# Kernel optimization log

Hardware: AMD Instinct MI355X
Metric: run time of the kernel (lower is better)

Reference implementation:

```python
import jax, jax.numpy as jnp
from jax import lax
import numpy as np

VAR0, VAR1 = 0.1, 0.2
K_TOP, T1, T2 = 5, 0.35, 0.5
ALPHA, GAMMA, BETA = 0.25, 2.0, 0.11


def point_form(b):
    # center form (cx,cy,w,h) -> corner form (x1,y1,x2,y2)
    return jnp.concatenate([b[:, :2] - b[:, 2:] / 2, b[:, :2] + b[:, 2:] / 2], axis=-1)


def jaccard(a, b):
    # a: [N,4], b: [P,4] corner boxes -> IoU [N,P]
    lt = jnp.maximum(a[:, None, :2], b[None, :, :2])
    rb = jnp.minimum(a[:, None, 2:], b[None, :, 2:])
    wh = jnp.clip(rb - lt, 0.0)
    inter = wh[..., 0] * wh[..., 1]
    area_a = ((a[:, 2] - a[:, 0]) * (a[:, 3] - a[:, 1]))[:, None]
    area_b = ((b[:, 2] - b[:, 0]) * (b[:, 3] - b[:, 1]))[None, :]
    return inter / (area_a + area_b - inter)


def encode(matched, priors):
    # matched: corner boxes [P,4], priors: center form [P,4]
    g_cxcy = ((matched[:, :2] + matched[:, 2:]) / 2 - priors[:, :2]) / (VAR0 * priors[:, 2:])
    g_wh = jnp.log((matched[:, 2:] - matched[:, :2]) / priors[:, 2:]) / VAR1
    return jnp.concatenate([g_cxcy, g_wh], axis=-1)


def decode(loc, priors):
    cxcy = priors[:, :2] + loc[:, :2] * VAR0 * priors[:, 2:]
    wh = priors[:, 2:] * jnp.exp(loc[:, 2:] * VAR1)
    return jnp.concatenate([cxcy - wh / 2, cxcy + wh / 2], axis=-1)


def _bce_logits(x, t):
    return jnp.maximum(x, 0.0) - x * t + jnp.log1p(jnp.exp(-jnp.abs(x)))


def focal_loss(logits, target, f_iou=None):
    C = logits.shape[-1]
    t = target.reshape(-1, 1)
    keep = (t >= 0.0).astype(logits.dtype)
    t = jnp.maximum(t, 0.0)
    pos = jnp.sum(t > 0.0).astype(logits.dtype)
    x = jnp.take_along_axis(logits.reshape(-1, C), t.astype(jnp.int32), axis=1)
    ce = _bce_logits(x, t)
    a = t * ALPHA + (1.0 - t) * (1.0 - ALPHA)
    p = jax.nn.sigmoid(x)
    pt = jnp.where(t == 1.0, p, 1.0 - p)
    if f_iou is not None:
        a = lax.stop_gradient(f_iou.reshape(-1, 1)) * a
    loss = a * (1.0 - pt) ** GAMMA * ce * keep
    return jnp.sum(loss) / jnp.maximum(pos, 1.0)


def smoothl1_masked(pred, target, mask):
    # equals SmoothL1Loss on the masked rows: sum(elem)/num_rows
    x = jnp.abs(pred - target)
    elem = jnp.where(x >= BETA, x - 0.5 * BETA, 0.5 * x * x / BETA)
    n = jnp.sum(mask).astype(pred.dtype)
    return jnp.sum(elem * mask[..., None].astype(pred.dtype)) / jnp.maximum(n, 1.0)


def match_image(loc_pred, tgt, priors_c, priors_pt):
    N = tgt.shape[0]
    P = priors_c.shape[0]
    truths = tgt[:, :4]
    labels = tgt[:, 4]
    iou = jaccard(truths, priors_pt)  # [N,P]
    bt_score = jnp.max(iou, axis=0)
    bt_idx = jnp.argmax(iou, axis=0).astype(jnp.int32)

    def greedy(_, st):
        m, s, ix = st
        flat = jnp.argmax(m)
        j = (flat // P).astype(jnp.int32)
        i = (flat % P).astype(jnp.int32)
        v = m.ravel()[flat]
        m = m.at[j, :].set(-1.0)
        m = m.at[:, i].set(-1.0)
        return (m, s.at[i].set(v), ix.at[i].set(j))

    _, bt_score, bt_idx = lax.fori_loop(0, N, greedy, (iou, bt_score, bt_idx))

    conf_s1 = labels[bt_idx]
    conf_s1 = jnp.where(bt_score < T1, 0.0, conf_s1)
    loc_s1 = encode(truths[bt_idx], priors_c)

    decoded = decode(lax.stop_gradient(loc_pred), priors_c)
    c_iou = jaccard(truths, decoded)  # [N,P]
    c_bp_score = jnp.max(c_iou, axis=0)
    c_bp_idx = jnp.argmax(c_iou, axis=0).astype(jnp.int32)
    c_iou = c_iou * (c_iou >= T2).astype(c_iou.dtype)
    tk_s, tk_i = lax.top_k(c_iou, K_TOP)  # per-truth top-K priors
    c_score = jnp.zeros_like(c_bp_score)

    def assign(t, st):
        cbi, cs = st
        i = (t // K_TOP).astype(jnp.int32)
        j = t % K_TOP
        p = tk_i[i, j]
        s = tk_s[i, j]
        cond = (conf_s1[p] < 1.0) & (s > 0.0)
        cbi = cbi.at[p].set(jnp.where(cond, i, cbi[p]))
        cs = cs.at[p].set(jnp.where(cond, s, cs[p]))
        return (cbi, cs)

    c_bp_idx, c_score = lax.fori_loop(0, N * K_TOP, assign, (c_bp_idx, c_score))

    loc_s2 = encode(truths[c_bp_idx], priors_c)
    conf_s2 = labels[c_bp_idx]
    conf_s2 = jnp.where(c_score < T2, -1.0, conf_s2)
    ignore = (bt_score < T1) & (c_bp_score >= T2) & (c_score < T2)
    conf_s1 = jnp.where(ignore, -1.0, conf_s1)
    return conf_s1, loc_s1, conf_s2, loc_s2, c_score


def setup_inputs() -> dict:
    key = jax.random.key(0)
    k1, k2, k3, k4, k5, k6 = jax.random.split(key, 6)
    B, P, N, C = 16, 102400, 32, 2
    loc_data = jax.random.normal(k1, (B, P, 4), jnp.float32)
    conf_data = jax.random.normal(k2, (B, P, C), jnp.float32)
    pcxy = jax.random.uniform(k3, (P, 2), jnp.float32, 0.0, 1.0)
    pwh = jax.random.uniform(k4, (P, 2), jnp.float32, 0.02, 0.25)
    priors = jnp.concatenate([pcxy, pwh], axis=-1)
    tcxy = jax.random.uniform(k5, (B, N, 2), jnp.float32, 0.1, 0.9)
    twh = jax.random.uniform(k6, (B, N, 2), jnp.float32, 0.05, 0.3)
    x1 = jnp.clip(tcxy - twh / 2, 0.0, 1.0)
    x2 = jnp.clip(tcxy + twh / 2, 0.0, 1.0)
    targets = jnp.concatenate([x1, x2, jnp.ones((B, N, 1), jnp.float32)], axis=-1)
    return {"loc_data": loc_data, "conf_data": conf_data, "priors": priors, "targets": targets}


def reference(loc_data, conf_data, priors, targets):
    priors_c = lax.stop_gradient(priors)  # torch uses priors.data
    tgts = lax.stop_gradient(targets)     # torch uses targets[idx].data
    priors_pt = point_form(priors_c)
    conf_t, loc_t, cconf_t, cloc_t, cc_score = jax.vmap(
        lambda lp, tg: match_image(lp, tg, priors_c, priors_pt))(loc_data, tgts)
    m1 = conf_t > 0.0
    m2 = cconf_t > 0.0
    n1 = jnp.sum(m1)
    n2 = jnp.sum(m2)
    l1 = smoothl1_masked(loc_data, loc_t, m1)
    l2 = smoothl1_masked(loc_data, cloc_t, m2)
    f1 = focal_loss(conf_data, conf_t, None)
    f2 = focal_loss(conf_data, cconf_t, cc_score)
    loc_loss = jnp.where(n1 > 0, l1, 0.0) + jnp.where(n2 > 0, l2, 0.0)
    cls_loss = jnp.where(n1 > 0, f1, 0.0) + jnp.where(n2 > 0, f2, 0.0)
    none_ = (n1 == 0) & (n2 == 0)
    return (jnp.where(none_, 1e-4, loc_loss), jnp.where(none_, 1e-4, cls_loss))
```

## Files before the change

kernel.cpp:

```cpp
#include <hip/hip_runtime.h>
#include <cstdint>
#include <cstddef>

#define VAR0_ 0.1f
#define VAR1_ 0.2f
#define KTOP_ 5
#define T1_ 0.35f
#define T2_ 0.5f
#define ALPHA_ 0.25f
#define BETA_ 0.11f
#define BS 256
#define BSK 128
#define NSPLIT 16
#define ILP 4

__device__ __forceinline__ float sl1(float d) {
    float x = fabsf(d);
    return (x >= BETA_) ? (x - 0.5f * BETA_) : (0.5f * x * x / BETA_);
}

__global__ void k_per_prior(const float4* __restrict__ loc4, const float4* __restrict__ priors4,
                            const float* __restrict__ targets,
                            float4* __restrict__ recs4,
                            float* __restrict__ cand_v, int* __restrict__ cand_i,
                            int* __restrict__ cand_cnt,
                            int P, int N, int CAP) {
    int b = blockIdx.y;
    int tid = threadIdx.x;
    int base = blockIdx.x * (BSK * ILP) + tid;
    __shared__ float4 tr4[64];
    __shared__ float trA[64];
    __shared__ float trT[64];
    for (int t = tid; t < N; t += BSK) {
        float x1 = targets[(size_t)(b * N + t) * 5 + 0];
        float y1 = targets[(size_t)(b * N + t) * 5 + 1];
        float x2 = targets[(size_t)(b * N + t) * 5 + 2];
        float y2 = targets[(size_t)(b * N + t) * 5 + 3];
        tr4[t] = make_float4(x1, y1, x2, y2);
        float a = (x2 - x1) * (y2 - y1);
        trA[t] = a;
        trT[t] = a * 0.33330f;
    }
    __syncthreads();
    if (base >= P) return;

    int iv[ILP]; int val[ILP];
    float px1[ILP], py1[ILP], px2[ILP], py2[ILP], pa[ILP];
#pragma unroll
    for (int k = 0; k < ILP; k++) {
        int i = base + k * BSK; iv[k] = i; val[k] = (i < P);
        float4 pr = val[k] ? priors4[i] : make_float4(0.f, 0.f, 1.f, 1.f);
        px1[k] = pr.x - pr.z * 0.5f; py1[k] = pr.y - pr.w * 0.5f;
        px2[k] = pr.x + pr.z * 0.5f; py2[k] = pr.y + pr.w * 0.5f;
        pa[k] = (px2[k] - px1[k]) * (py2[k] - py1[k]);
    }

    float bi[ILP], bu[ILP]; int bn[ILP];
#pragma unroll
    for (int k = 0; k < ILP; k++) { bi[k] = -1.f; bu[k] = 1.f; bn[k] = 0; }
#pragma unroll 2
    for (int n = 0; n < N; n++) {
        float4 t4 = tr4[n];
        float ta = trA[n];
#pragma unroll
        for (int k = 0; k < ILP; k++) {
            float lx = fmaxf(t4.x, px1[k]), ly = fmaxf(t4.y, py1[k]);
            float rx = fminf(t4.z, px2[k]), ry = fminf(t4.w, py2[k]);
            float w = fmaxf(rx - lx, 0.f), h = fmaxf(ry - ly, 0.f);
            float inter = w * h, uni = ta + pa[k] - inter;
            bool bet = inter * bu[k] > bi[k] * uni;
            bi[k] = bet ? inter : bi[k]; bu[k] = bet ? uni : bu[k]; bn[k] = bet ? n : bn[k];
        }
    }
    float bv[ILP];
#pragma unroll
    for (int k = 0; k < ILP; k++) bv[k] = bi[k] / bu[k];

    float dx1[ILP], dy1[ILP], dx2[ILP], dy2[ILP], da[ILP], daC[ILP];
#pragma unroll
    for (int k = 0; k < ILP; k++) {
        float4 pr = val[k] ? priors4[iv[k]] : make_float4(0.f, 0.f, 1.f, 1.f);
        float4 lc = val[k] ? loc4[(size_t)b * P + iv[k]] : make_float4(0.f, 0.f, 0.f, 0.f);
        float dcx = pr.x + lc.x * VAR0_ * pr.z;
        float dcy = pr.y + lc.y * VAR0_ * pr.w;
        float dw = pr.z * expf(lc.z * VAR1_);
        float dh = pr.w * expf(lc.w * VAR1_);
        dx1[k] = dcx - dw * 0.5f; dy1[k] = dcy - dh * 0.5f;
        dx2[k] = dcx + dw * 0.5f; dy2[k] = dcy + dh * 0.5f;
        da[k] = (dx2[k] - dx1[k]) * (dy2[k] - dy1[k]);
        daC[k] = da[k] * 0.33330f;
    }
    unsigned long long hm[ILP];
#pragma unroll
    for (int k = 0; k < ILP; k++) hm[k] = 0ull;
#pragma unroll 2
    for (int n = 0; n < N; n++) {
        float4 t4 = tr4[n];
        float tt = trT[n];
#pragma unroll
        for (int k = 0; k < ILP; k++) {
            float lx = fmaxf(t4.x, dx1[k]), ly = fmaxf(t4.y, dy1[k]);
            float rx = fminf(t4.z, dx2[k]), ry = fminf(t4.w, dy2[k]);
            float w = fmaxf(rx - lx, 0.f), h = fmaxf(ry - ly, 0.f);
            float inter = w * h;
            if (inter >= tt + daC[k]) hm[k] |= (1ull << n);
        }
    }

#pragma unroll
    for (int k = 0; k < ILP; k++) {
        if (!val[k]) continue;
        int had = 0;
        unsigned long long m = hm[k];
        while (m) {
            int n = __ffsll((long long)m) - 1;
            m &= m - 1;
            float4 t4 = tr4[n];
            float lx = fmaxf(t4.x, dx1[k]), ly = fmaxf(t4.y, dy1[k]);
            float rx = fminf(t4.z, dx2[k]), ry = fminf(t4.w, dy2[k]);
            float w = fmaxf(rx - lx, 0.f), h = fmaxf(ry - ly, 0.f);
            float inter = w * h;
            float v = inter / (trA[n] + da[k] - inter);
            if (v >= T2_) {
                had = 1;
                int pos = atomicAdd(&cand_cnt[b * N + n], 1);
                if (pos < CAP) {
                    size_t o = (size_t)(b * N + n) * CAP + pos;
                    cand_v[o] = v; cand_i[o] = iv[k];
                }
            }
        }
        recs4[(size_t)b * P + iv[k]] =
            make_float4(bv[k], __int_as_float(bn[k] | (had << 16)), __int_as_float(0), 0.f);
    }
}

__global__ void k_row_max_part(const float4* __restrict__ priors4, const float* __restrict__ targets,
                               float* __restrict__ part_max, int* __restrict__ part_arg,
                               int P, int N) {
    int s = blockIdx.x, b = blockIdx.y, g = blockIdx.z;
    int n0 = g * 4;
    int chunk = (P + NSPLIT - 1) / NSPLIT;
    int i0 = s * chunk;
    int i1 = min(P, i0 + chunk);
    float tx1[4], ty1[4], tx2[4], ty2[4], ta[4];
#pragma unroll
    for (int k = 0; k < 4; k++) {
        int n = min(n0 + k, N - 1);
        tx1[k] = targets[(size_t)(b * N + n) * 5 + 0];
        ty1[k] = targets[(size_t)(b * N + n) * 5 + 1];
        tx2[k] = targets[(size_t)(b * N + n) * 5 + 2];
        ty2[k] = targets[(size_t)(b * N + n) * 5 + 3];
        ta[k] = (tx2[k] - tx1[k]) * (ty2[k] - ty1[k]);
    }
    float cI[4], cU[4]; int cX[4];
#pragma unroll
    for (int k = 0; k < 4; k++) { cI[k] = -1.f; cU[k] = 1.f; cX[k] = 0x7fffffff; }
    for (int i = i0 + threadIdx.x; i < i1; i += BS) {
        float4 pr = priors4[i];
        float px1 = pr.x - pr.z * 0.5f, py1 = pr.y - pr.w * 0.5f;
        float px2 = pr.x + pr.z * 0.5f, py2 = pr.y + pr.w * 0.5f;
        float pa = (px2 - px1) * (py2 - py1);
#pragma unroll
        for (int k = 0; k < 4; k++) {
            float lx = fmaxf(tx1[k], px1), ly = fmaxf(ty1[k], py1);
            float rx = fminf(tx2[k], px2), ry = fminf(ty2[k], py2);
            float w = fmaxf(rx - lx, 0.f), h = fmaxf(ry - ly, 0.f);
            float inter = w * h;
            float uni = ta[k] + pa - inter;
            bool bet = inter * cU[k] > cI[k] * uni;
            cI[k] = bet ? inter : cI[k]; cU[k] = bet ? uni : cU[k]; cX[k] = bet ? i : cX[k];
        }
    }
    int tid = threadIdx.x;
    int lane = tid & 63, wid = tid >> 6;
    __shared__ float swv[BS / 64];
    __shared__ int swi[BS / 64];
#pragma unroll
    for (int k = 0; k < 4; k++) {
        if (n0 + k >= N) break;
        float bv = cI[k] / cU[k];
        int bx = cX[k];
#pragma unroll
        for (int off = 32; off > 0; off >>= 1) {
            float ov = __shfl_xor(bv, off);
            int oi = __shfl_xor(bx, off);
            if (ov > bv || (ov == bv && oi < bx)) { bv = ov; bx = oi; }
        }
        if (lane == 0) { swv[wid] = bv; swi[wid] = bx; }
        __syncthreads();
        if (tid == 0) {
            float fv = swv[0]; int fi = swi[0];
            for (int wv = 1; wv < BS / 64; wv++) {
                if (swv[wv] > fv || (swv[wv] == fv && swi[wv] < fi)) { fv = swv[wv]; fi = swi[wv]; }
            }
            int o = (b * N + (n0 + k)) * NSPLIT + s;
            part_max[o] = fv; part_arg[o] = fi;
        }
        __syncthreads();
    }
}

__global__ void k_greedy(const float4* __restrict__ priors4, const float* __restrict__ targets,
                         const float* __restrict__ part_max, const int* __restrict__ part_arg,
                         float* __restrict__ recs, int P, int N) {
    int b = blockIdx.x;
    int lane = threadIdx.x;
    extern __shared__ unsigned int mask[];
    int maskWords = (P + 31) >> 5;
    for (int w = lane; w < maskWords; w += 64) mask[w] = 0u;

    float rmax = -2.f; int rarg = 0x7fffffff; int alive = 0;
    float tx1 = 0.f, ty1 = 0.f, tx2 = 0.f, ty2 = 0.f, ta = 0.f;
    if (lane < N) {
        float bv = -2.f; int bi = 0x7fffffff;
        for (int s = 0; s < NSPLIT; s++) {
            int o = (b * N + lane) * NSPLIT + s;
            float v = part_max[o]; int ix = part_arg[o];
            if (v > bv || (v == bv && ix < bi)) { bv = v; bi = ix; }
        }
        rmax = bv; rarg = bi;
        alive = 1;
        tx1 = targets[(size_t)(b * N + lane) * 5 + 0];
        ty1 = targets[(size_t)(b * N + lane) * 5 + 1];
        tx2 = targets[(size_t)(b * N + lane) * 5 + 2];
        ty2 = targets[(size_t)(b * N + lane) * 5 + 3];
        ta = (tx2 - tx1) * (ty2 - ty1);
    }
    __syncthreads();

    for (int it = 0; it < N; it++) {
        float v = (lane < N && alive) ? rmax : -3.f;
        int idx = lane;
#pragma unroll
        for (int off = 32; off > 0; off >>= 1) {
            float ov = __shfl_xor(v, off);
            int oi = __shfl_xor(idx, off);
            if (ov > v || (ov == v && oi < idx)) { v = ov; idx = oi; }
        }
        int bj = idx;
        float bv = v;
        int sel = __shfl(rarg, bj);
        if (lane == bj) alive = 0;
        if (lane == 0) {
            float* base = recs + 4 * ((size_t)b * P + sel);
            int wrd = __float_as_int(base[1]);
            base[0] = bv;
            base[1] = __int_as_float((wrd & ~0xFFFF) | bj);
            mask[sel >> 5] |= (1u << (sel & 31));
        }
        __syncthreads();

        unsigned long long coll = __ballot(lane < N && alive && rarg == sel);
        while (coll) {
            int r = __ffsll((long long)coll) - 1;
            coll &= coll - 1;
            float rx1 = __shfl(tx1, r), ry1 = __shfl(ty1, r);
            float rx2 = __shfl(tx2, r), ry2 = __shfl(ty2, r);
            float ra = __shfl(ta, r);
            float n_i = -2.f, n_u = 1.f; int ni = 0x7fffffff;
            for (int i = lane; i < P; i += 64) {
                if (mask[i >> 5] & (1u << (i & 31))) continue;
                float4 pr = priors4[i];
                float px1 = pr.x - pr.z * 0.5f, py1 = pr.y - pr.w * 0.5f;
                float px2 = pr.x + pr.z * 0.5f, py2 = pr.y + pr.w * 0.5f;
                float lx = fmaxf(rx1, px1), ly = fmaxf(ry1, py1);
                float rx = fminf(rx2, px2), ry = fminf(ry2, py2);
                float w = fmaxf(rx - lx, 0.f), h = fmaxf(ry - ly, 0.f);
                float inter = w * h;
                float uni = ra + (px2 - px1) * (py2 - py1) - inter;
                bool better = inter * n_u > n_i * uni;
                n_i = better ? inter : n_i; n_u = better ? uni : n_u; ni = better ? i : ni;
            }
            float nv = n_i / n_u;
#pragma unroll
            for (int off = 32; off > 0; off >>= 1) {
                float ov = __shfl_xor(nv, off);
                int oi = __shfl_xor(ni, off);
                if (ov > nv || (ov == nv && oi < ni)) { nv = ov; ni = oi; }
            }
            if (lane == r) { rmax = nv; rarg = ni; }
        }
        __syncthreads();
    }
}

__global__ void k_topk(const float4* __restrict__ loc4, const float4* __restrict__ priors4,
                       const float* __restrict__ targets,
                       const float* __restrict__ cand_v, const int* __restrict__ cand_i,
                       const int* __restrict__ cand_cnt,
                       float* __restrict__ tk_s, int* __restrict__ tk_i,
                       int P, int N, int CAP) {
    int n = blockIdx.x, b = blockIdx.y;
    int row = b * N + n;
    int tid = threadIdx.x;

    float vals[KTOP_]; int ids[KTOP_];
#pragma unroll
    for (int k = 0; k < KTOP_; k++) { vals[k] = -1.f; ids[k] = 0x7fffffff; }

    int cnt = cand_cnt[row];
    if (cnt <= CAP) {
        for (int k = tid; k < cnt; k += blockDim.x) {
            float cv = cand_v[(size_t)row * CAP + k];
            int ci = cand_i[(size_t)row * CAP + k];
#pragma unroll
            for (int q = 0; q < KTOP_; q++) {
                bool better = (cv > vals[q]) || ((cv == vals[q]) && (ci < ids[q]));
                float tv = better ? cv : vals[q]; int ti = better ? ci : ids[q];
                cv = better ? vals[q] : cv; ci = better ? ids[q] : ci;
                vals[q] = tv; ids[q] = ti;
            }
        }
    } else {
        float tx1 = targets[(size_t)row * 5 + 0], ty1 = targets[(size_t)row * 5 + 1];
        float tx2 = targets[(size_t)row * 5 + 2], ty2 = targets[(size_t)row * 5 + 3];
        float ta = (tx2 - tx1) * (ty2 - ty1);
        for (int i = tid; i < P; i += blockDim.x) {
            float4 pr = priors4[i];
            size_t bp = (size_t)b * P + i;
            float4 lc = loc4[bp];
            float dcx = pr.x + lc.x * VAR0_ * pr.z;
            float dcy = pr.y + lc.y * VAR0_ * pr.w;
            float dw = pr.z * expf(lc.z * VAR1_);
            float dh = pr.w * expf(lc.w * VAR1_);
            float dx1 = dcx - dw * 0.5f, dy1 = dcy - dh * 0.5f;
            float dx2 = dcx + dw * 0.5f, dy2 = dcy + dh * 0.5f;
            float lx = fmaxf(tx1, dx1), ly = fmaxf(ty1, dy1);
            float rx = fminf(tx2, dx2), ry = fminf(ty2, dy2);
            float w = fmaxf(rx - lx, 0.f), h = fmaxf(ry - ly, 0.f);
            float inter = w * h;
            float uni = ta + (dx2 - dx1) * (dy2 - dy1) - inter;
            if (inter >= uni * 0.4999990f) {
                float v = inter / uni;
                if (v >= T2_) {
                    float cv = v; int ci = i;
#pragma unroll
                    for (int q = 0; q < KTOP_; q++) {
                        bool better = (cv > vals[q]) || ((cv == vals[q]) && (ci < ids[q]));
                        float tv = better ? cv : vals[q]; int ti = better ? ci : ids[q];
                        cv = better ? vals[q] : cv; ci = better ? ids[q] : ci;
                        vals[q] = tv; ids[q] = ti;
                    }
                }
            }
        }
    }

    __shared__ float mv[BS * KTOP_];
    __shared__ int mi[BS * KTOP_];
#pragma unroll
    for (int k = 0; k < KTOP_; k++) { mv[tid * KTOP_ + k] = vals[k]; mi[tid * KTOP_ + k] = ids[k]; }
    __syncthreads();
    for (int s = BS / 2; s > 0; s >>= 1) {
        if (tid < s) {
#pragma unroll
            for (int j = 0; j < KTOP_; j++) {
                float cv = mv[(tid + s) * KTOP_ + j];
                int ci = mi[(tid + s) * KTOP_ + j];
#pragma unroll
                for (int q = 0; q < KTOP_; q++) {
                    bool better = (cv > vals[q]) || ((cv == vals[q]) && (ci < ids[q]));
                    float tv = better ? cv : vals[q]; int ti = better ? ci : ids[q];
                    cv = better ? vals[q] : cv; ci = better ? ids[q] : ci;
                    vals[q] = tv; ids[q] = ti;
                }
            }
#pragma unroll
            for (int k = 0; k < KTOP_; k++) { mv[tid * KTOP_ + k] = vals[k]; mi[tid * KTOP_ + k] = ids[k]; }
        }
        __syncthreads();
    }
    if (tid == 0) {
#pragma unroll
        for (int k = 0; k < KTOP_; k++) {
            tk_s[(size_t)row * KTOP_ + k] = (vals[k] > 0.f) ? vals[k] : 0.f;
            tk_i[(size_t)row * KTOP_ + k] = (ids[k] == 0x7fffffff) ? 0 : ids[k];
        }
    }
}

__global__ void k_assign(const float* __restrict__ targets,
                         const float* __restrict__ tk_s, const int* __restrict__ tk_i,
                         float* __restrict__ recs, int P, int N) {
    int b = blockIdx.x;
    int tid = threadIdx.x;
    int T = N * KTOP_;
    __shared__ int sh_p[512];
    __shared__ float sh_s[512];
    __shared__ int sh_c[512];
    if (tid < T) {
        int i = tid / KTOP_, j = tid % KTOP_;
        int p = tk_i[(size_t)(b * N + i) * KTOP_ + j];
        float s = tk_s[(size_t)(b * N + i) * KTOP_ + j];
        const float* base = recs + 4 * ((size_t)b * P + p);
        float bs = base[0];
        int bj = __float_as_int(base[1]) & 0xFFFF;
        float conf1 = (bs < T1_) ? 0.f : targets[(size_t)(b * N + bj) * 5 + 4];
        sh_p[tid] = p; sh_s[tid] = s;
        sh_c[tid] = (conf1 < 1.f && s > 0.f) ? 1 : 0;
    }
    __syncthreads();
    if (tid < T && sh_c[tid]) {
        int p = sh_p[tid];
        bool last = true;
        for (int t2 = tid + 1; t2 < T; t2++) {
            if (sh_c[t2] && sh_p[t2] == p) { last = false; break; }
        }
        if (last) {
            float* base = recs + 4 * ((size_t)b * P + p);
            base[2] = __int_as_float(tid / KTOP_);
            base[3] = sh_s[tid];
        }
    }
}

__global__ void k_loss(const float4* __restrict__ loc4, const float* __restrict__ conf,
                       const float4* __restrict__ priors4, const float* __restrict__ targets,
                       const float4* __restrict__ recs4,
                       double* __restrict__ partials,
                       int P, int N, int C) {
    int b = blockIdx.y;
    int i = blockIdx.x * blockDim.x + threadIdx.x;
    double l1 = 0.0, l2 = 0.0, f1 = 0.0, f2 = 0.0;
    int n1 = 0, n2 = 0;
    if (i < P) {
        size_t bp = (size_t)b * P + i;
        float4 r = recs4[bp];
        float bs = r.x;
        int widx = __float_as_int(r.y);
        int bj = widx & 0xFFFF;
        int hadCand = (widx >> 16) & 1;
        float cs = r.w;
        int cj = (cs > 0.f) ? __float_as_int(r.z) : 0;
        float lab1 = targets[(size_t)(b * N + bj) * 5 + 4];
        float conf1 = (bs < T1_) ? 0.f : lab1;
        if ((bs < T1_) && hadCand && (cs < T2_)) conf1 = -1.f;
        float lab2 = targets[(size_t)(b * N + cj) * 5 + 4];
        float conf2 = (cs < T2_) ? -1.f : lab2;
        bool m1 = conf1 > 0.f, m2 = conf2 > 0.f;
        n1 = m1 ? 1 : 0; n2 = m2 ? 1 : 0;

        if (m1 || m2) {
            float4 pr = priors4[i];
            float pcx = pr.x, pcy = pr.y, pw = pr.z, ph = pr.w;
            float4 lc = loc4[bp];
            float p0 = lc.x, p1 = lc.y, p2 = lc.z, p3 = lc.w;
            if (m1) {
                const float* tb = &targets[(size_t)(b * N + bj) * 5];
                float gx = ((tb[0] + tb[2]) * 0.5f - pcx) / (VAR0_ * pw);
                float gy = ((tb[1] + tb[3]) * 0.5f - pcy) / (VAR0_ * ph);
                float gw = logf((tb[2] - tb[0]) / pw) / VAR1_;
                float gh = logf((tb[3] - tb[1]) / ph) / VAR1_;
                l1 = (double)(sl1(p0 - gx) + sl1(p1 - gy) + sl1(p2 - gw) + sl1(p3 - gh));
            }
            if (m2) {
                const float* tb = &targets[(size_t)(b * N + cj) * 5];
                float gx = ((tb[0] + tb[2]) * 0.5f - pcx) / (VAR0_ * pw);
                float gy = ((tb[1] + tb[3]) * 0.5f - pcy) / (VAR0_ * ph);
                float gw = logf((tb[2] - tb[0]) / pw) / VAR1_;
                float gh = logf((tb[3] - tb[1]) / ph) / VAR1_;
                l2 = (double)(sl1(p0 - gx) + sl1(p1 - gy) + sl1(p2 - gw) + sl1(p3 - gh));
            }
        }
        float x0, x1v;
        if (C == 2) {
            float2 cv2 = ((const float2*)conf)[bp];
            x0 = cv2.x; x1v = cv2.y;
        } else {
            x0 = conf[bp * C + 0]; x1v = conf[bp * C + 1];
        }
        {
            float t = fmaxf(conf1, 0.f);
            float keep = (conf1 >= 0.f) ? 1.f : 0.f;
            float x = (t >= 1.f) ? x1v : x0;
            float ce = fmaxf(x, 0.f) - x * t + log1pf(expf(-fabsf(x)));
            float a = t * ALPHA_ + (1.f - t) * (1.f - ALPHA_);
            float pr_ = 1.f / (1.f + expf(-x));
            float pt = (t == 1.f) ? pr_ : (1.f - pr_);
            float om = 1.f - pt;
            f1 = (double)(a * om * om * ce * keep);
        }
        {
            float t = fmaxf(conf2, 0.f);
            float keep = (conf2 >= 0.f) ? 1.f : 0.f;
            float x = (t >= 1.f) ? x1v : x0;
            float ce = fmaxf(x, 0.f) - x * t + log1pf(expf(-fabsf(x)));
            float a = cs * (t * ALPHA_ + (1.f - t) * (1.f - ALPHA_));
            float pr_ = 1.f / (1.f + expf(-x));
            float pt = (t == 1.f) ? pr_ : (1.f - pr_);
            float om = 1.f - pt;
            f2 = (double)(a * om * om * ce * keep);
        }
    }
    int tid = threadIdx.x;
    int lane = tid & 63, wid = tid >> 6;
#pragma unroll
    for (int off = 32; off > 0; off >>= 1) {
        l1 += __shfl_xor(l1, off);
        l2 += __shfl_xor(l2, off);
        f1 += __shfl_xor(f1, off);
        f2 += __shfl_xor(f2, off);
        n1 += __shfl_xor(n1, off);
        n2 += __shfl_xor(n2, off);
    }
    __shared__ double swd[BS / 64][4];
    __shared__ int swn[BS / 64][2];
    if (lane == 0) {
        swd[wid][0] = l1; swd[wid][1] = l2; swd[wid][2] = f1; swd[wid][3] = f2;
        swn[wid][0] = n1; swn[wid][1] = n2;
    }
    __syncthreads();
    if (tid == 0) {
        double a0 = 0, a1 = 0, a2 = 0, a3 = 0; int b0 = 0, b1 = 0;
        for (int wv = 0; wv < BS / 64; wv++) {
            a0 += swd[wv][0]; a1 += swd[wv][1]; a2 += swd[wv][2]; a3 += swd[wv][3];
            b0 += swn[wv][0]; b1 += swn[wv][1];
        }
        int blk = blockIdx.y * gridDim.x + blockIdx.x;
        partials[(size_t)blk * 6 + 0] = a0;
        partials[(size_t)blk * 6 + 1] = a1;
        partials[(size_t)blk * 6 + 2] = a2;
        partials[(size_t)blk * 6 + 3] = a3;
        partials[(size_t)blk * 6 + 4] = (double)b0;
        partials[(size_t)blk * 6 + 5] = (double)b1;
    }
}

__global__ void k_final(const double* __restrict__ partials, int nPart, float* __restrict__ out) {
    int tid = threadIdx.x;
    double a[6] = {0, 0, 0, 0, 0, 0};
    for (int k = tid; k < nPart; k += BS) {
#pragma unroll
        for (int j = 0; j < 6; j++) a[j] += partials[(size_t)k * 6 + j];
    }
    __shared__ double sd[BS * 6];
#pragma unroll
    for (int j = 0; j < 6; j++) sd[tid * 6 + j] = a[j];
    __syncthreads();
    for (int s = BS / 2; s > 0; s >>= 1) {
        if (tid < s) {
#pragma unroll
            for (int j = 0; j < 6; j++) sd[tid * 6 + j] += sd[(tid + s) * 6 + j];
        }
        __syncthreads();
    }
    if (tid == 0) {
        double L1 = sd[0], L2 = sd[1], F1 = sd[2], F2 = sd[3], N1 = sd[4], N2 = sd[5];
        double l1v = L1 / fmax(N1, 1.0), l2v = L2 / fmax(N2, 1.0);
        double f1v = F1 / fmax(N1, 1.0), f2v = F2 / fmax(N2, 1.0);
        double locl = (N1 > 0 ? l1v : 0.0) + (N2 > 0 ? l2v : 0.0);
        double clsl = (N1 > 0 ? f1v : 0.0) + (N2 > 0 ? f2v : 0.0);
        if (N1 == 0 && N2 == 0) { locl = 1e-4; clsl = 1e-4; }
        out[0] = (float)locl;
        out[1] = (float)clsl;
    }
}

extern "C" void kernel_launch(void* const* d_in, const int* in_sizes, int n_in,
                              void* d_out, int out_size, void* d_ws, size_t ws_size,
                              hipStream_t stream) {
    const float* targets = (const float*)d_in[3];
    const float* conf = (const float*)d_in[1];
    const float4* loc4 = (const float4*)d_in[0];
    const float4* priors4 = (const float4*)d_in[2];

    int P = in_sizes[2] / 4;
    int B = in_sizes[0] / (P * 4);
    int N = in_sizes[3] / (B * 5);
    int C = in_sizes[1] / (B * P);
    const int CAP = 2048;
    size_t BP = (size_t)B * P;

    unsigned char* ws = (unsigned char*)d_ws;
    size_t off = 0;
    auto alloc = [&](size_t bytes) { size_t cur = off; off += (bytes + 255) & ~(size_t)255; return cur; };
    float* recs = (float*)(ws + alloc(BP * 16));
    float* part_max = (float*)(ws + alloc((size_t)B * N * NSPLIT * 4));
    int* part_arg = (int*)(ws + alloc((size_t)B * N * NSPLIT * 4));
    float* tk_s = (float*)(ws + alloc((size_t)B * N * KTOP_ * 4));
    int* tk_i = (int*)(ws + alloc((size_t)B * N * KTOP_ * 4));
    float* cand_v = (float*)(ws + alloc((size_t)B * N * CAP * 4));
    int* cand_i = (int*)(ws + alloc((size_t)B * N * CAP * 4));
    int* cand_cnt = (int*)(ws + alloc((size_t)B * N * 4));
    int bx = (P + BS - 1) / BS;
    double* partials = (double*)(ws + alloc((size_t)bx * B * 6 * 8));
    float* out = (float*)d_out;

    hipMemsetAsync(cand_cnt, 0, (size_t)B * N * 4, stream);
    int bx4 = (P + BSK * ILP - 1) / (BSK * ILP);
    k_per_prior<<<dim3(bx4, B), BSK, 0, stream>>>(loc4, priors4, targets, (float4*)recs,
                                                  cand_v, cand_i, cand_cnt, P, N, CAP);
    int ngroup = (N + 3) / 4;
    k_row_max_part<<<dim3(NSPLIT, B, ngroup), BS, 0, stream>>>(priors4, targets,
                                                               part_max, part_arg, P, N);
    int maskWords = (P + 31) / 32;
    size_t shmem = (size_t)maskWords * 4;
    k_greedy<<<dim3(B), 64, shmem, stream>>>(priors4, targets, part_max, part_arg,
                                             recs, P, N);
    k_topk<<<dim3(N, B), BS, 0, stream>>>(loc4, priors4, targets, cand_v, cand_i, cand_cnt,
                                          tk_s, tk_i, P, N, CAP);
    k_assign<<<dim3(B), BS, 0, stream>>>(targets, tk_s, tk_i, recs, P, N);
    k_loss<<<dim3(bx, B), BS, 0, stream>>>(loc4, conf, priors4, targets, (const float4*)recs,
                                           partials, P, N, C);
    k_final<<<1, BS, 0, stream>>>(partials, bx * B, out);
}
```

Measured before the change: 213.6 us.

## Fuse greedy, top-k and assign kernels; fold final reduction into loss kernel

```diff
diff --git a/kernel.cpp b/kernel.cpp
--- a/kernel.cpp
+++ b/kernel.cpp
@@ -17,6 +17,11 @@
 __device__ __forceinline__ float sl1(float d) {
     float x = fabsf(d);
     return (x >= BETA_) ? (x - 0.5f * BETA_) : (0.5f * x * x / BETA_);
+}
+
+__global__ void k_init(int* __restrict__ cand_cnt, int nCnt) {
+    int i = blockIdx.x * blockDim.x + threadIdx.x;
+    if (i < nCnt) cand_cnt[i] = 0;
 }
 
 __global__ void k_per_prior(const float4* __restrict__ loc4, const float4* __restrict__ priors4,
@@ -106,7 +111,6 @@
             if (inter >= tt + daC[k]) hm[k] |= (1ull << n);
         }
     }
-
 #pragma unroll
     for (int k = 0; k < ILP; k++) {
         if (!val[k]) continue;
@@ -201,18 +205,30 @@
     }
 }
 
-__global__ void k_greedy(const float4* __restrict__ priors4, const float* __restrict__ targets,
-                         const float* __restrict__ part_max, const int* __restrict__ part_arg,
-                         float* __restrict__ recs, int P, int N) {
+__global__ void k_combo(const float4* __restrict__ loc4, const float4* __restrict__ priors4,
+                        const float* __restrict__ targets,
+                        const float* __restrict__ part_max, const int* __restrict__ part_arg,
+                        const float* __restrict__ cand_v, const int* __restrict__ cand_i,
+                        const int* __restrict__ cand_cnt,
+                        float* __restrict__ recs,
+                        int P, int N, int CAP) {
     int b = blockIdx.x;
-    int lane = threadIdx.x;
+    int tid = threadIdx.x;
+    int lane = tid & 63, wid = tid >> 6;
     extern __shared__ unsigned int mask[];
+    __shared__ float mv[BS * KTOP_];
+    __shared__ int mi[BS * KTOP_];
+    __shared__ float sh_tks[64 * KTOP_];
+    __shared__ int sh_tki[64 * KTOP_];
+    __shared__ int sh_p[64 * KTOP_];
+    __shared__ int sh_c[64 * KTOP_];
+
     int maskWords = (P + 31) >> 5;
-    for (int w = lane; w < maskWords; w += 64) mask[w] = 0u;
+    for (int w = tid; w < maskWords; w += BS) mask[w] = 0u;
 
     float rmax = -2.f; int rarg = 0x7fffffff; int alive = 0;
     float tx1 = 0.f, ty1 = 0.f, tx2 = 0.f, ty2 = 0.f, ta = 0.f;
-    if (lane < N) {
+    if (wid == 0 && lane < N) {
         float bv = -2.f; int bi = 0x7fffffff;
         for (int s = 0; s < NSPLIT; s++) {
             int o = (b * N + lane) * NSPLIT + s;
@@ -230,111 +246,125 @@
     __syncthreads();
 
     for (int it = 0; it < N; it++) {
-        float v = (lane < N && alive) ? rmax : -3.f;
-        int idx = lane;
-#pragma unroll
-        for (int off = 32; off > 0; off >>= 1) {
-            float ov = __shfl_xor(v, off);
-            int oi = __shfl_xor(idx, off);
-            if (ov > v || (ov == v && oi < idx)) { v = ov; idx = oi; }
-        }
-        int bj = idx;
-        float bv = v;
-        int sel = __shfl(rarg, bj);
-        if (lane == bj) alive = 0;
-        if (lane == 0) {
-            float* base = recs + 4 * ((size_t)b * P + sel);
-            int wrd = __float_as_int(base[1]);
-            base[0] = bv;
-            base[1] = __int_as_float((wrd & ~0xFFFF) | bj);
-            mask[sel >> 5] |= (1u << (sel & 31));
+        int sel = 0;
+        if (wid == 0) {
+            float v = (lane < N && alive) ? rmax : -3.f;
+            int idx = lane;
+#pragma unroll
+            for (int off = 32; off > 0; off >>= 1) {
+                float ov = __shfl_xor(v, off);
+                int oi = __shfl_xor(idx, off);
+                if (ov > v || (ov == v && oi < idx)) { v = ov; idx = oi; }
+            }
+            int bj = idx;
+            float bv = v;
+            sel = __shfl(rarg, bj);
+            if (lane == bj) alive = 0;
+            if (lane == 0) {
+                float* base = recs + 4 * ((size_t)b * P + sel);
+                int wrd = __float_as_int(base[1]);
+                base[0] = bv;
+                base[1] = __int_as_float((wrd & ~0xFFFF) | bj);
+                mask[sel >> 5] |= (1u << (sel & 31));
+            }
         }
         __syncthreads();
-
-        unsigned long long coll = __ballot(lane < N && alive && rarg == sel);
-        while (coll) {
-            int r = __ffsll((long long)coll) - 1;
-            coll &= coll - 1;
-            float rx1 = __shfl(tx1, r), ry1 = __shfl(ty1, r);
-            float rx2 = __shfl(tx2, r), ry2 = __shfl(ty2, r);
-            float ra = __shfl(ta, r);
-            float n_i = -2.f, n_u = 1.f; int ni = 0x7fffffff;
-            for (int i = lane; i < P; i += 64) {
-                if (mask[i >> 5] & (1u << (i & 31))) continue;
+        if (wid == 0) {
+            unsigned long long coll = __ballot(lane < N && alive && rarg == sel);
+            while (coll) {
+                int r = __ffsll((long long)coll) - 1;
+                coll &= coll - 1;
+                float rx1 = __shfl(tx1, r), ry1 = __shfl(ty1, r);
+                float rx2 = __shfl(tx2, r), ry2 = __shfl(ty2, r);
+                float ra = __shfl(ta, r);
+                float n_i = -2.f, n_u = 1.f; int ni = 0x7fffffff;
+                for (int i = lane; i < P; i += 64) {
+                    if (mask[i >> 5] & (1u << (i & 31))) continue;
+                    float4 pr = priors4[i];
+                    float px1 = pr.x - pr.z * 0.5f, py1 = pr.y - pr.w * 0.5f;
+                    float px2 = pr.x + pr.z * 0.5f, py2 = pr.y + pr.w * 0.5f;
+                    float lx = fmaxf(rx1, px1), ly = fmaxf(ry1, py1);
+                    float rx = fminf(rx2, px2), ry = fminf(ry2, py2);
+                    float w = fmaxf(rx - lx, 0.f), h = fmaxf(ry - ly, 0.f);
+                    float inter = w * h;
+                    float uni = ra + (px2 - px1) * (py2 - py1) - inter;
+                    bool better = inter * n_u > n_i * uni;
+                    n_i = better ? inter : n_i; n_u = better ? uni : n_u; ni = better ? i : ni;
+                }
+                float nv = n_i / n_u;
+#pragma unroll
+                for (int off = 32; off > 0; off >>= 1) {
+                    float ov = __shfl_xor(nv, off);
+                    int oi = __shfl_xor(ni, off);
+                    if (ov > nv || (ov == nv && oi < ni)) { nv = ov; ni = oi; }
+                }
+                if (lane == r) { rmax = nv; rarg = ni; }
+            }
+        }
+        __syncthreads();
+    }
+
+    for (int n = 0; n < N; n++) {
+        int row = b * N + n;
+        float vals[KTOP_]; int ids[KTOP_];
+#pragma unroll
+        for (int k = 0; k < KTOP_; k++) { vals[k] = -1.f; ids[k] = 0x7fffffff; }
+        int cnt = cand_cnt[row];
+        if (cnt <= CAP) {
+            for (int k = tid; k < cnt; k += BS) {
+                float cv = cand_v[(size_t)row * CAP + k];
+                int ci = cand_i[(size_t)row * CAP + k];
+#pragma unroll
+                for (int q = 0; q < KTOP_; q++) {
+                    bool better = (cv > vals[q]) || ((cv == vals[q]) && (ci < ids[q]));
+                    float tv = better ? cv : vals[q]; int ti = better ? ci : ids[q];
+                    cv = better ? vals[q] : cv; ci = better ? ids[q] : ci;
+                    vals[q] = tv; ids[q] = ti;
+                }
+            }
+        } else {
+            float qx1 = targets[(size_t)row * 5 + 0], qy1 = targets[(size_t)row * 5 + 1];
+            float qx2 = targets[(size_t)row * 5 + 2], qy2 = targets[(size_t)row * 5 + 3];
+            float qa = (qx2 - qx1) * (qy2 - qy1);
+            for (int i = tid; i < P; i += BS) {
                 float4 pr = priors4[i];
-                float px1 = pr.x - pr.z * 0.5f, py1 = pr.y - pr.w * 0.5f;
-                float px2 = pr.x + pr.z * 0.5f, py2 = pr.y + pr.w * 0.5f;
-                float lx = fmaxf(rx1, px1), ly = fmaxf(ry1, py1);
-                float rx = fminf(rx2, px2), ry = fminf(ry2, py2);
+                size_t bp = (size_t)b * P + i;
+                float4 lc = loc4[bp];
+                float dcx = pr.x + lc.x * VAR0_ * pr.z;
+                float dcy = pr.y + lc.y * VAR0_ * pr.w;
+                float dw = pr.z * expf(lc.z * VAR1_);
+                float dh = pr.w * expf(lc.w * VAR1_);
+                float dx1 = dcx - dw * 0.5f, dy1 = dcy - dh * 0.5f;
+                float dx2 = dcx + dw * 0.5f, dy2 = dcy + dh * 0.5f;
+                float lx = fmaxf(qx1, dx1), ly = fmaxf(qy1, dy1);
+                float rx = fminf(qx2, dx2), ry = fminf(qy2, dy2);
                 float w = fmaxf(rx - lx, 0.f), h = fmaxf(ry - ly, 0.f);
                 float inter = w * h;
-                float uni = ra + (px2 - px1) * (py2 - py1) - inter;
-                bool better = inter * n_u > n_i * uni;
-                n_i = better ? inter : n_i; n_u = better ? uni : n_u; ni = better ? i : ni;
-            }
-            float nv = n_i / n_u;
-#pragma unroll
-            for (int off = 32; off > 0; off >>= 1) {
-                float ov = __shfl_xor(nv, off);
-                int oi = __shfl_xor(ni, off);
-                if (ov > nv || (ov == nv && oi < ni)) { nv = ov; ni = oi; }
-            }
-            if (lane == r) { rmax = nv; rarg = ni; }
-        }
+                float uni = qa + (dx2 - dx1) * (dy2 - dy1) - inter;
+                if (inter >= uni * 0.4999990f) {
+                    float v = inter / uni;
+                    if (v >= T2_) {
+                        float cv = v; int ci = i;
+#pragma unroll
+                        for (int q = 0; q < KTOP_; q++) {
+                            bool better = (cv > vals[q]) || ((cv == vals[q]) && (ci < ids[q]));
+                            float tv = better ? cv : vals[q]; int ti = better ? ci : ids[q];
+                            cv = better ? vals[q] : cv; ci = better ? ids[q] : ci;
+                            vals[q] = tv; ids[q] = ti;
+                        }
+                    }
+                }
+            }
+        }
+#pragma unroll
+        for (int k = 0; k < KTOP_; k++) { mv[tid * KTOP_ + k] = vals[k]; mi[tid * KTOP_ + k] = ids[k]; }
         __syncthreads();
-    }
-}
-
-__global__ void k_topk(const float4* __restrict__ loc4, const float4* __restrict__ priors4,
-                       const float* __restrict__ targets,
-                       const float* __restrict__ cand_v, const int* __restrict__ cand_i,
-                       const int* __restrict__ cand_cnt,
-                       float* __restrict__ tk_s, int* __restrict__ tk_i,
-                       int P, int N, int CAP) {
-    int n = blockIdx.x, b = blockIdx.y;
-    int row = b * N + n;
-    int tid = threadIdx.x;
-
-    float vals[KTOP_]; int ids[KTOP_];
-#pragma unroll
-    for (int k = 0; k < KTOP_; k++) { vals[k] = -1.f; ids[k] = 0x7fffffff; }
-
-    int cnt = cand_cnt[row];
-    if (cnt <= CAP) {
-        for (int k = tid; k < cnt; k += blockDim.x) {
-            float cv = cand_v[(size_t)row * CAP + k];
-            int ci = cand_i[(size_t)row * CAP + k];
-#pragma unroll
-            for (int q = 0; q < KTOP_; q++) {
-                bool better = (cv > vals[q]) || ((cv == vals[q]) && (ci < ids[q]));
-                float tv = better ? cv : vals[q]; int ti = better ? ci : ids[q];
-                cv = better ? vals[q] : cv; ci = better ? ids[q] : ci;
-                vals[q] = tv; ids[q] = ti;
-            }
-        }
-    } else {
-        float tx1 = targets[(size_t)row * 5 + 0], ty1 = targets[(size_t)row * 5 + 1];
-        float tx2 = targets[(size_t)row * 5 + 2], ty2 = targets[(size_t)row * 5 + 3];
-        float ta = (tx2 - tx1) * (ty2 - ty1);
-        for (int i = tid; i < P; i += blockDim.x) {
-            float4 pr = priors4[i];
-            size_t bp = (size_t)b * P + i;
-            float4 lc = loc4[bp];
-            float dcx = pr.x + lc.x * VAR0_ * pr.z;
-            float dcy = pr.y + lc.y * VAR0_ * pr.w;
-            float dw = pr.z * expf(lc.z * VAR1_);
-            float dh = pr.w * expf(lc.w * VAR1_);
-            float dx1 = dcx - dw * 0.5f, dy1 = dcy - dh * 0.5f;
-            float dx2 = dcx + dw * 0.5f, dy2 = dcy + dh * 0.5f;
-            float lx = fmaxf(tx1, dx1), ly = fmaxf(ty1, dy1);
-            float rx = fminf(tx2, dx2), ry = fminf(ty2, dy2);
-            float w = fmaxf(rx - lx, 0.f), h = fmaxf(ry - ly, 0.f);
-            float inter = w * h;
-            float uni = ta + (dx2 - dx1) * (dy2 - dy1) - inter;
-            if (inter >= uni * 0.4999990f) {
-                float v = inter / uni;
-                if (v >= T2_) {
-                    float cv = v; int ci = i;
+        for (int s = BS / 2; s > 0; s >>= 1) {
+            if (tid < s) {
+#pragma unroll
+                for (int j = 0; j < KTOP_; j++) {
+                    float cv = mv[(tid + s) * KTOP_ + j];
+                    int ci = mi[(tid + s) * KTOP_ + j];
 #pragma unroll
                     for (int q = 0; q < KTOP_; q++) {
                         bool better = (cv > vals[q]) || ((cv == vals[q]) && (ci < ids[q]));
@@ -343,61 +373,30 @@
                         vals[q] = tv; ids[q] = ti;
                     }
                 }
-            }
-        }
-    }
-
-    __shared__ float mv[BS * KTOP_];
-    __shared__ int mi[BS * KTOP_];
-#pragma unroll
-    for (int k = 0; k < KTOP_; k++) { mv[tid * KTOP_ + k] = vals[k]; mi[tid * KTOP_ + k] = ids[k]; }
-    __syncthreads();
-    for (int s = BS / 2; s > 0; s >>= 1) {
-        if (tid < s) {
-#pragma unroll
-            for (int j = 0; j < KTOP_; j++) {
-                float cv = mv[(tid + s) * KTOP_ + j];
-                int ci = mi[(tid + s) * KTOP_ + j];
-#pragma unroll
-                for (int q = 0; q < KTOP_; q++) {
-                    bool better = (cv > vals[q]) || ((cv == vals[q]) && (ci < ids[q]));
-                    float tv = better ? cv : vals[q]; int ti = better ? ci : ids[q];
-                    cv = better ? vals[q] : cv; ci = better ? ids[q] : ci;
-                    vals[q] = tv; ids[q] = ti;
-                }
-            }
-#pragma unroll
-            for (int k = 0; k < KTOP_; k++) { mv[tid * KTOP_ + k] = vals[k]; mi[tid * KTOP_ + k] = ids[k]; }
+#pragma unroll
+                for (int k = 0; k < KTOP_; k++) { mv[tid * KTOP_ + k] = vals[k]; mi[tid * KTOP_ + k] = ids[k]; }
+            }
+            __syncthreads();
+        }
+        if (tid == 0) {
+#pragma unroll
+            for (int k = 0; k < KTOP_; k++) {
+                sh_tks[n * KTOP_ + k] = (vals[k] > 0.f) ? vals[k] : 0.f;
+                sh_tki[n * KTOP_ + k] = (ids[k] == 0x7fffffff) ? 0 : ids[k];
+            }
         }
         __syncthreads();
     }
-    if (tid == 0) {
-#pragma unroll
-        for (int k = 0; k < KTOP_; k++) {
-            tk_s[(size_t)row * KTOP_ + k] = (vals[k] > 0.f) ? vals[k] : 0.f;
-            tk_i[(size_t)row * KTOP_ + k] = (ids[k] == 0x7fffffff) ? 0 : ids[k];
-        }
-    }
-}
-
-__global__ void k_assign(const float* __restrict__ targets,
-                         const float* __restrict__ tk_s, const int* __restrict__ tk_i,
-                         float* __restrict__ recs, int P, int N) {
-    int b = blockIdx.x;
-    int tid = threadIdx.x;
+
     int T = N * KTOP_;
-    __shared__ int sh_p[512];
-    __shared__ float sh_s[512];
-    __shared__ int sh_c[512];
     if (tid < T) {
-        int i = tid / KTOP_, j = tid % KTOP_;
-        int p = tk_i[(size_t)(b * N + i) * KTOP_ + j];
-        float s = tk_s[(size_t)(b * N + i) * KTOP_ + j];
+        int p = sh_tki[tid];
+        float s = sh_tks[tid];
         const float* base = recs + 4 * ((size_t)b * P + p);
         float bs = base[0];
         int bj = __float_as_int(base[1]) & 0xFFFF;
         float conf1 = (bs < T1_) ? 0.f : targets[(size_t)(b * N + bj) * 5 + 4];
-        sh_p[tid] = p; sh_s[tid] = s;
+        sh_p[tid] = p;
         sh_c[tid] = (conf1 < 1.f && s > 0.f) ? 1 : 0;
     }
     __syncthreads();
@@ -410,16 +409,17 @@
         if (last) {
             float* base = recs + 4 * ((size_t)b * P + p);
             base[2] = __int_as_float(tid / KTOP_);
-            base[3] = sh_s[tid];
+            base[3] = sh_tks[tid];
         }
     }
 }
 
-__global__ void k_loss(const float4* __restrict__ loc4, const float* __restrict__ conf,
-                       const float4* __restrict__ priors4, const float* __restrict__ targets,
-                       const float4* __restrict__ recs4,
-                       double* __restrict__ partials,
-                       int P, int N, int C) {
+__global__ void k_loss_final(const float4* __restrict__ loc4, const float* __restrict__ conf,
+                             const float4* __restrict__ priors4, const float* __restrict__ targets,
+                             const float4* __restrict__ recs4,
+                             double* __restrict__ partials, int* __restrict__ done_cnt,
+                             float* __restrict__ out,
+                             int P, int N, int C, int nPart) {
     int b = blockIdx.y;
     int i = blockIdx.x * blockDim.x + threadIdx.x;
     double l1 = 0.0, l2 = 0.0, f1 = 0.0, f2 = 0.0;
@@ -440,7 +440,6 @@
         float conf2 = (cs < T2_) ? -1.f : lab2;
         bool m1 = conf1 > 0.f, m2 = conf2 > 0.f;
         n1 = m1 ? 1 : 0; n2 = m2 ? 1 : 0;
-
         if (m1 || m2) {
             float4 pr = priors4[i];
             float pcx = pr.x, pcy = pr.y, pw = pr.z, ph = pr.w;
@@ -511,6 +510,7 @@
         swn[wid][0] = n1; swn[wid][1] = n2;
     }
     __syncthreads();
+    __shared__ int s_last;
     if (tid == 0) {
         double a0 = 0, a1 = 0, a2 = 0, a3 = 0; int b0 = 0, b1 = 0;
         for (int wv = 0; wv < BS / 64; wv++) {
@@ -524,36 +524,39 @@
         partials[(size_t)blk * 6 + 3] = a3;
         partials[(size_t)blk * 6 + 4] = (double)b0;
         partials[(size_t)blk * 6 + 5] = (double)b1;
-    }
-}
-
-__global__ void k_final(const double* __restrict__ partials, int nPart, float* __restrict__ out) {
-    int tid = threadIdx.x;
-    double a[6] = {0, 0, 0, 0, 0, 0};
-    for (int k = tid; k < nPart; k += BS) {
-#pragma unroll
-        for (int j = 0; j < 6; j++) a[j] += partials[(size_t)k * 6 + j];
-    }
-    __shared__ double sd[BS * 6];
-#pragma unroll
-    for (int j = 0; j < 6; j++) sd[tid * 6 + j] = a[j];
+        __threadfence();
+        int prev = atomicAdd(done_cnt, 1);
+        s_last = (prev == nPart - 1) ? 1 : 0;
+    }
     __syncthreads();
-    for (int s = BS / 2; s > 0; s >>= 1) {
-        if (tid < s) {
-#pragma unroll
-            for (int j = 0; j < 6; j++) sd[tid * 6 + j] += sd[(tid + s) * 6 + j];
-        }
+    if (s_last) {
+        __threadfence();
+        double a[6] = {0, 0, 0, 0, 0, 0};
+        for (int k = tid; k < nPart; k += BS) {
+#pragma unroll
+            for (int j = 0; j < 6; j++) a[j] += partials[(size_t)k * 6 + j];
+        }
+        __shared__ double sd[BS * 6];
+#pragma unroll
+        for (int j = 0; j < 6; j++) sd[tid * 6 + j] = a[j];
         __syncthreads();
-    }
-    if (tid == 0) {
-        double L1 = sd[0], L2 = sd[1], F1 = sd[2], F2 = sd[3], N1 = sd[4], N2 = sd[5];
-        double l1v = L1 / fmax(N1, 1.0), l2v = L2 / fmax(N2, 1.0);
-        double f1v = F1 / fmax(N1, 1.0), f2v = F2 / fmax(N2, 1.0);
-        double locl = (N1 > 0 ? l1v : 0.0) + (N2 > 0 ? l2v : 0.0);
-        double clsl = (N1 > 0 ? f1v : 0.0) + (N2 > 0 ? f2v : 0.0);
-        if (N1 == 0 && N2 == 0) { locl = 1e-4; clsl = 1e-4; }
-        out[0] = (float)locl;
-        out[1] = (float)clsl;
+        for (int s = BS / 2; s > 0; s >>= 1) {
+            if (tid < s) {
+#pragma unroll
+                for (int j = 0; j < 6; j++) sd[tid * 6 + j] += sd[(tid + s) * 6 + j];
+            }
+            __syncthreads();
+        }
+        if (tid == 0) {
+            double L1 = sd[0], L2 = sd[1], F1 = sd[2], F2 = sd[3], N1 = sd[4], N2 = sd[5];
+            double l1v = L1 / fmax(N1, 1.0), l2v = L2 / fmax(N2, 1.0);
+            double f1v = F1 / fmax(N1, 1.0), f2v = F2 / fmax(N2, 1.0);
+            double locl = (N1 > 0 ? l1v : 0.0) + (N2 > 0 ? l2v : 0.0);
+            double clsl = (N1 > 0 ? f1v : 0.0) + (N2 > 0 ? f2v : 0.0);
+            if (N1 == 0 && N2 == 0) { locl = 1e-4; clsl = 1e-4; }
+            out[0] = (float)locl;
+            out[1] = (float)clsl;
+        }
     }
 }
 
@@ -578,16 +581,16 @@
     float* recs = (float*)(ws + alloc(BP * 16));
     float* part_max = (float*)(ws + alloc((size_t)B * N * NSPLIT * 4));
     int* part_arg = (int*)(ws + alloc((size_t)B * N * NSPLIT * 4));
-    float* tk_s = (float*)(ws + alloc((size_t)B * N * KTOP_ * 4));
-    int* tk_i = (int*)(ws + alloc((size_t)B * N * KTOP_ * 4));
     float* cand_v = (float*)(ws + alloc((size_t)B * N * CAP * 4));
     int* cand_i = (int*)(ws + alloc((size_t)B * N * CAP * 4));
-    int* cand_cnt = (int*)(ws + alloc((size_t)B * N * 4));
+    int* cand_cnt = (int*)(ws + alloc(((size_t)B * N + 1) * 4));
     int bx = (P + BS - 1) / BS;
     double* partials = (double*)(ws + alloc((size_t)bx * B * 6 * 8));
     float* out = (float*)d_out;
-
-    hipMemsetAsync(cand_cnt, 0, (size_t)B * N * 4, stream);
+    int* done_cnt = cand_cnt + B * N;
+
+    k_init<<<dim3((B * N + 1 + BS - 1) / BS), dim3(BS), 0, stream>>>(cand_cnt, B * N + 1);
+
     int bx4 = (P + BSK * ILP - 1) / (BSK * ILP);
     k_per_prior<<<dim3(bx4, B), BSK, 0, stream>>>(loc4, priors4, targets, (float4*)recs,
                                                   cand_v, cand_i, cand_cnt, P, N, CAP);
@@ -596,12 +599,9 @@
                                                                part_max, part_arg, P, N);
     int maskWords = (P + 31) / 32;
     size_t shmem = (size_t)maskWords * 4;
-    k_greedy<<<dim3(B), 64, shmem, stream>>>(priors4, targets, part_max, part_arg,
-                                             recs, P, N);
-    k_topk<<<dim3(N, B), BS, 0, stream>>>(loc4, priors4, targets, cand_v, cand_i, cand_cnt,
-                                          tk_s, tk_i, P, N, CAP);
-    k_assign<<<dim3(B), BS, 0, stream>>>(targets, tk_s, tk_i, recs, P, N);
-    k_loss<<<dim3(bx, B), BS, 0, stream>>>(loc4, conf, priors4, targets, (const float4*)recs,
-                                           partials, P, N, C);
-    k_final<<<1, BS, 0, stream>>>(partials, bx * B, out);
+    k_combo<<<dim3(B), BS, shmem, stream>>>(loc4, priors4, targets, part_max, part_arg,
+                                            cand_v, cand_i, cand_cnt, recs, P, N, CAP);
+    k_loss_final<<<dim3(bx, B), BS, 0, stream>>>(loc4, conf, priors4, targets,
+                                                 (const float4*)recs, partials, done_cnt,
+                                                 out, P, N, C, bx * B);
 }
```

New measurement: 729.8 us. 242% more time.
